# Performance work log

Hardware: AMD Instinct MI355X
Metric: run time of the kernel (lower is better)

The kernel has to match this reference:

```python
import jax, jax.numpy as jnp
import numpy as np

R = 256   # resolution
C = 16    # n_chan
F = 8     # n_freq
N = 262144


def setup_inputs() -> dict:
    key = jax.random.key(0)
    k1, k2 = jax.random.split(key)
    coords = jax.random.uniform(k1, (N, 3), dtype=jnp.float32, minval=-1.0, maxval=1.0)
    grid = jax.random.normal(k2, (3, C * F, R, R), dtype=jnp.float32) * 0.1
    # matches torch init: linspace(0,1,C*F).reshape(-1,C).T.reshape(-1)
    freqs = jnp.linspace(0.0, 1.0, C * F, dtype=jnp.float32).reshape(-1, C).T.reshape(-1)
    return {"coords": coords, "grid": grid, "freqs": freqs}


def _reflect(x, size):
    # PyTorch grid_sample reflection padding, align_corners=True:
    # reflect unnormalized coords about [0, size-1], period 2*(size-1)
    span = size - 1
    m = 2 * span
    r = jnp.abs(x) % m
    return jnp.where(r > span, m - r, r)


def _grid_sample_plane(img, xy):
    # img: (CF, R, R); xy: (Npts, 2) normalized [-1,1], (x indexes W, y indexes H)
    ix = _reflect((xy[:, 0] + 1.0) * 0.5 * (R - 1), R)
    iy = _reflect((xy[:, 1] + 1.0) * 0.5 * (R - 1), R)
    x0f = jnp.floor(ix); y0f = jnp.floor(iy)
    wx = ix - x0f; wy = iy - y0f
    x0 = jnp.clip(x0f.astype(jnp.int32), 0, R - 1)
    x1 = jnp.clip(x0 + 1, 0, R - 1)
    y0 = jnp.clip(y0f.astype(jnp.int32), 0, R - 1)
    y1 = jnp.clip(y0 + 1, 0, R - 1)
    v00 = img[:, y0, x0]  # (CF, Npts)
    v01 = img[:, y0, x1]
    v10 = img[:, y1, x0]
    v11 = img[:, y1, x1]
    return (v00 * (1 - wx) * (1 - wy) + v01 * wx * (1 - wy)
            + v10 * (1 - wx) * wy + v11 * wx * wy)


def reference(coords, grid, freqs):
    n = coords.shape[0]
    # tri-plane sample coords: plane0 (y,z), plane1 (x,z), plane2 (x,y)
    xy = jnp.stack([coords[:, (1, 2)], coords[:, (0, 2)], coords[:, (0, 1)]], 0)  # (3,N,2)
    coefs = jax.vmap(_grid_sample_plane)(grid, xy)          # (3, CF, N)
    coefs = coefs.transpose(2, 1, 0).reshape(n, C, F, 3)    # (N, C, F, 3)
    # get_freqs(): 2**(clamp(freqs,0,1)*log2(R)) - 1
    fr = 2.0 ** (jnp.clip(freqs, 0.0, 1.0) * np.float32(np.log2(R))) - 1.0  # (CF,)
    pts = (coords + 1.0) * 0.5 * (R - 1)                    # (N, 3)
    phase = (jnp.pi / R) * (pts[:, None, None, :] + 0.5) * (fr.reshape(C, F)[None, :, :, None] + 0.5)
    basis = jnp.cos(phase)                                   # (N, C, F, 3)
    # einsum BCFT,BCFT->BCT then sum over T == sum over (F, T)
    return 2.0 * jnp.sum(coefs * basis, axis=(2, 3))         # (N, C)
```

## Files before the change

### kernel.cpp

```cpp
#include <hip/hip_runtime.h>

#define RES   256
#define NCH   128
#define NC    16
#define QG    32
#define NPK   64
#define NBINS 4096
#define TBLK  3072

typedef float fx2 __attribute__((ext_vector_type(2)));

__device__ __forceinline__ unsigned int f32_to_bf16_rne(float f) {
    unsigned int u = __float_as_uint(f);
    return (u + 0x7FFFu + ((u >> 16) & 1u)) >> 16;
}
__device__ __forceinline__ float bf16_lo(unsigned int w) {
    return __uint_as_float(w << 16);
}
__device__ __forceinline__ float bf16_hi(unsigned int w) {
    return __uint_as_float(w & 0xFFFF0000u);
}
__device__ __forceinline__ float reflectf(float v) {
    float r = fabsf(v);
    r = fmodf(r, 510.0f);
    return (r > 255.0f) ? (510.0f - r) : r;
}
__device__ __forceinline__ unsigned spread3(unsigned v) {
    return (v & 1u) | ((v & 2u) << 2) | ((v & 4u) << 4) | ((v & 8u) << 6);
}
__device__ __forceinline__ int point_cell(const float* __restrict__ coords, int i) {
    const float r0 = reflectf((coords[3 * (size_t)i + 0] + 1.0f) * 127.5f);
    const float r1 = reflectf((coords[3 * (size_t)i + 1] + 1.0f) * 127.5f);
    const float r2 = reflectf((coords[3 * (size_t)i + 2] + 1.0f) * 127.5f);
    const unsigned cx = (unsigned)min(max((int)r0, 0), 255) >> 4;
    const unsigned cy = (unsigned)min(max((int)r1, 0), 255) >> 4;
    const unsigned cz = (unsigned)min(max((int)r2, 0), 255) >> 4;
    return (int)(spread3(cx) | (spread3(cy) << 1) | (spread3(cz) << 2));
}

__global__ __launch_bounds__(256) void fg_transpose_hist(
    const float* __restrict__ in, unsigned int* __restrict__ out,
    const float* __restrict__ coords, unsigned* __restrict__ hist, int n)
{
    __shared__ unsigned int tile[QG / 2][RES + 4];
    const int tid = threadIdx.x;
    const int qg = blockIdx.x;
    const int y  = blockIdx.y;
    const int p  = blockIdx.z;

    {
        const int bid = (p * RES + y) * 4 + qg;
        const int per = (n + TBLK - 1) / TBLK;
        const int s0 = bid * per;
        const int s1 = min(s0 + per, n);
        for (int k = s0 + tid; k < s1; k += 256)
            atomicAdd(&hist[point_cell(coords, k)], 1u);
    }

    const int q0 = qg * QG;
    const float* src = in + (((size_t)p * NCH + q0) * RES + y) * RES;
    #pragma unroll
    for (int it = 0; it < 4; ++it) {
        const int lin = it * 256 + tid;
        const int k   = lin >> 6;
        const int x4  = lin & 63;
        const float4 a = *(const float4*)(src + (size_t)(2 * k + 0) * (RES * RES) + x4 * 4);
        const float4 b = *(const float4*)(src + (size_t)(2 * k + 1) * (RES * RES) + x4 * 4);
        uint4 w;
        w.x = f32_to_bf16_rne(a.x) | (f32_to_bf16_rne(b.x) << 16);
        w.y = f32_to_bf16_rne(a.y) | (f32_to_bf16_rne(b.y) << 16);
        w.z = f32_to_bf16_rne(a.z) | (f32_to_bf16_rne(b.z) << 16);
        w.w = f32_to_bf16_rne(a.w) | (f32_to_bf16_rne(b.w) << 16);
        *(uint4*)&tile[k][x4 * 4] = w;
    }
    __syncthreads();
    unsigned int* dst = out + (((size_t)p * RES + y) * RES) * NPK + (q0 >> 1);
    #pragma unroll
    for (int it = 0; it < 4; ++it) {
        const int lin = it * 256 + tid;
        const int q4 = lin & 3;
        const int x  = lin >> 2;
        uint4 w;
        w.x = tile[4 * q4 + 0][x];
        w.y = tile[4 * q4 + 1][x];
        w.z = tile[4 * q4 + 2][x];
        w.w = tile[4 * q4 + 3][x];
        *(uint4*)&dst[(size_t)x * NPK + q4 * 4] = w;
    }
}

__global__ __launch_bounds__(256) void fg_scan(
    const unsigned* __restrict__ hist, unsigned* __restrict__ cursor,
    const float* __restrict__ freqs, float* __restrict__ frp)
{
    __shared__ unsigned wtot[4];
    const int t = threadIdx.x;
    const int lane = t & 63;
    const int wid = t >> 6;
    unsigned loc[16];
    unsigned sum = 0;
    #pragma unroll
    for (int k = 0; k < 16; ++k) { loc[k] = hist[t * 16 + k]; sum += loc[k]; }
    unsigned v = sum;
    #pragma unroll
    for (int off = 1; off < 64; off <<= 1) {
        unsigned u = __shfl_up(v, off);
        if (lane >= off) v += u;
    }
    if (lane == 63) wtot[wid] = v;
    __syncthreads();
    unsigned base = 0;
    #pragma unroll
    for (int w = 0; w < 4; ++w) base += (w < wid) ? wtot[w] : 0u;
    unsigned run = base + (v - sum);
    #pragma unroll
    for (int k = 0; k < 16; ++k) { cursor[t * 16 + k] = run; run += loc[k]; }
    if (t < 128) {
        const float f = fminf(fmaxf(freqs[t], 0.0f), 1.0f);
        frp[t] = __builtin_amdgcn_exp2f(f * 8.0f) - 0.5f;
    }
}

__global__ __launch_bounds__(256) void fg_scatter(
    const float* __restrict__ coords, unsigned* __restrict__ cursor,
    float4* __restrict__ recP, unsigned* __restrict__ idx, int n)
{
    const int i = blockIdx.x * 256 + threadIdx.x;
    if (i >= n) return;
    const float c0 = coords[3 * (size_t)i + 0];
    const float c1 = coords[3 * (size_t)i + 1];
    const float c2 = coords[3 * (size_t)i + 2];
    const float p0 = (c0 + 1.0f) * 127.5f;
    const float p1 = (c1 + 1.0f) * 127.5f;
    const float p2 = (c2 + 1.0f) * 127.5f;
    const float r0 = reflectf(p0);
    const float r1 = reflectf(p1);
    const float r2 = reflectf(p2);
    const unsigned cx = (unsigned)min(max((int)r0, 0), 255) >> 4;
    const unsigned cy = (unsigned)min(max((int)r1, 0), 255) >> 4;
    const unsigned cz = (unsigned)min(max((int)r2, 0), 255) >> 4;
    const int cell = (int)(spread3(cx) | (spread3(cy) << 1) | (spread3(cz) << 2));
    const unsigned pos = atomicAdd(&cursor[cell], 1u);

    #pragma unroll
    for (int p = 0; p < 3; ++p) {
        const float ix = (p == 0) ? r1 : r0;
        const float iy = (p == 2) ? r1 : r2;
        const float pp = (p == 0) ? p0 : ((p == 1) ? p1 : p2);
        const float x0f = floorf(ix), y0f = floorf(iy);
        const float wx = ix - x0f, wy = iy - y0f;
        const int x0 = min(max((int)x0f, 0), RES - 1);
        const int y0 = min(max((int)y0f, 0), RES - 1);
        unsigned ob = (unsigned)(((p << 16) | (y0 << 8) | x0) << 6);
        if (x0 < RES - 1) ob |= (1u << 24);
        if (y0 < RES - 1) ob |= (1u << 25);
        const float A = (pp + 0.5f) * (1.0f / 512.0f);
        recP[(size_t)pos * 3 + p] = make_float4(A, wx, wy, __uint_as_float(ob));
    }
    idx[pos] = (unsigned)i;
}

__global__ __launch_bounds__(256) void fg_main_bf16(
    const unsigned int* __restrict__ grid,
    const float* __restrict__ frp_in,
    const float4* __restrict__ recP,
    const unsigned* __restrict__ idx,
    float* __restrict__ out, int n)
{
    const int t = threadIdx.x;
    const int c = t & 15;
    int b = blockIdx.x;
    {
        const int G = gridDim.x;
        const int chunk = G >> 3;
        const int lim = chunk << 3;
        if (b < lim) b = (b & 7) * chunk + (b >> 3);
    }
    const int slot = b * 16 + (t >> 4);
    if (slot >= n) return;

    float4 P[3];
    P[0] = recP[(size_t)slot * 3 + 0];
    P[1] = recP[(size_t)slot * 3 + 1];
    P[2] = recP[(size_t)slot * 3 + 2];
    const unsigned i = idx[slot];

    fx2 frpv[4];
    {
        float frp[8];
        *(float4*)(frp + 0) = *(const float4*)(frp_in + c * 8 + 0);
        *(float4*)(frp + 4) = *(const float4*)(frp_in + c * 8 + 4);
        #pragma unroll
        for (int jj = 0; jj < 4; ++jj) {
            frpv[jj].x = frp[2 * jj + 0];
            frpv[jj].y = frp[2 * jj + 1];
        }
    }

    const int c4 = c * 4;
    uint4 g[3][4];
    #pragma unroll
    for (int p = 0; p < 3; ++p) {
        const unsigned bits = __float_as_uint(P[p].w);
        const int base = (int)(bits & 0x00FFFFFFu) + c4;
        const int dx = (int)((bits >> 18) & 64u);
        const int dy = (int)((bits >> 11) & 16384u);
        g[p][0] = *(const uint4*)(grid + base);
        g[p][1] = *(const uint4*)(grid + base + dx);
        g[p][2] = *(const uint4*)(grid + base + dy);
        g[p][3] = *(const uint4*)(grid + base + dx + dy);
    }

    fx2 acc2 = {0.0f, 0.0f};
    #pragma unroll
    for (int p = 0; p < 3; ++p) {
        const float wx = P[p].y, wy = P[p].z;
        const float u = 1.0f - wx, v = 1.0f - wy;
        const float w00 = u * v,  w01 = wx * v;
        const float w10 = u * wy, w11 = wx * wy;
        const float A = P[p].x;
        const unsigned int w0[4] = {g[p][0].x, g[p][0].y, g[p][0].z, g[p][0].w};
        const unsigned int w1[4] = {g[p][1].x, g[p][1].y, g[p][1].z, g[p][1].w};
        const unsigned int w2[4] = {g[p][2].x, g[p][2].y, g[p][2].z, g[p][2].w};
        const unsigned int w3[4] = {g[p][3].x, g[p][3].y, g[p][3].z, g[p][3].w};

        #pragma unroll
        for (int jj = 0; jj < 4; ++jj) {
            fx2 v0; v0.x = bf16_lo(w0[jj]); v0.y = bf16_hi(w0[jj]);
            fx2 v1; v1.x = bf16_lo(w1[jj]); v1.y = bf16_hi(w1[jj]);
            fx2 v2; v2.x = bf16_lo(w2[jj]); v2.y = bf16_hi(w2[jj]);
            fx2 v3; v3.x = bf16_lo(w3[jj]); v3.y = bf16_hi(w3[jj]);
            const fx2 cf = w00 * v0 + w01 * v1 + w10 * v2 + w11 * v3;
            fx2 ph = A * frpv[jj];
            ph.x = __builtin_amdgcn_fractf(ph.x);
            ph.y = __builtin_amdgcn_fractf(ph.y);
            fx2 cs;
            cs.x = __builtin_amdgcn_cosf(ph.x);
            cs.y = __builtin_amdgcn_cosf(ph.y);
            acc2 += cf * cs;
        }
    }

    __builtin_nontemporal_store(2.0f * (acc2.x + acc2.y), &out[(size_t)i * NC + c]);
}

__global__ __launch_bounds__(256) void fg_main_f32(
    const float* __restrict__ coords,
    const float* __restrict__ grid,
    const float* __restrict__ freqs,
    float* __restrict__ out, int n)
{
    const int t = threadIdx.x;
    const int c = t & 15;
    const int i = blockIdx.x * 16 + (t >> 4);
    if (i >= n) return;

    float frp[8];
    #pragma unroll
    for (int j = 0; j < 8; ++j) {
        float f = fminf(fmaxf(freqs[c * 8 + j], 0.0f), 1.0f);
        frp[j] = __builtin_amdgcn_exp2f(f * 8.0f) - 0.5f;
    }
    const float c0 = coords[3 * (size_t)i + 0];
    const float c1 = coords[3 * (size_t)i + 1];
    const float c2 = coords[3 * (size_t)i + 2];
    const float pts0 = (c0 + 1.0f) * 127.5f;
    const float pts1 = (c1 + 1.0f) * 127.5f;
    const float pts2 = (c2 + 1.0f) * 127.5f;
    float acc = 0.0f;
    #pragma unroll
    for (int p = 0; p < 3; ++p) {
        const float sx = (p == 0) ? pts1 : pts0;
        const float sy = (p == 2) ? pts1 : pts2;
        const float pp = (p == 0) ? pts0 : ((p == 1) ? pts1 : pts2);
        const float ix = reflectf(sx);
        const float iy = reflectf(sy);
        const float x0f = floorf(ix), y0f = floorf(iy);
        const float wx = ix - x0f, wy = iy - y0f;
        int x0 = (int)x0f; x0 = min(max(x0, 0), RES - 1);
        int y0 = (int)y0f; y0 = min(max(y0, 0), RES - 1);
        const int x1 = min(x0 + 1, RES - 1);
        const int y1 = min(y0 + 1, RES - 1);
        const float w00 = (1.0f - wx) * (1.0f - wy);
        const float w01 = wx * (1.0f - wy);
        const float w10 = (1.0f - wx) * wy;
        const float w11 = wx * wy;
        const float A = (pp + 0.5f) * (1.0f / 512.0f);
        const size_t plane = (size_t)p * NCH * RES * RES;
        const int o00 = y0 * RES + x0, o01 = y0 * RES + x1;
        const int o10 = y1 * RES + x0, o11 = y1 * RES + x1;
        #pragma unroll
        for (int j = 0; j < 8; ++j) {
            const float* gq = grid + plane + (size_t)(c * 8 + j) * (RES * RES);
            const float coef = w00 * gq[o00] + w01 * gq[o01]
                             + w10 * gq[o10] + w11 * gq[o11];
            const float rr = __builtin_amdgcn_fractf(A * frp[j]);
            acc += coef * __builtin_amdgcn_cosf(rr);
        }
    }
    out[(size_t)i * NC + c] = 2.0f * acc;
}

extern "C" void kernel_launch(void* const* d_in, const int* in_sizes, int n_in,
                              void* d_out, int out_size, void* d_ws, size_t ws_size,
                              hipStream_t stream)
{
    const float* coords = (const float*)d_in[0];
    const float* grid   = (const float*)d_in[1];
    const float* freqs  = (const float*)d_in[2];
    float* out = (float*)d_out;
    const int n = in_sizes[0] / 3;

    const size_t gridT_b  = (size_t)3 * RES * RES * NPK * sizeof(unsigned);
    const size_t hist_b   = (size_t)NBINS * sizeof(unsigned);
    const size_t frp_b    = 128 * sizeof(float);
    const size_t recP_b   = (size_t)n * 3 * sizeof(float4);
    const size_t idx_b    = (size_t)((n + 3) & ~3) * sizeof(unsigned);
    const size_t need = gridT_b + 2 * hist_b + frp_b + recP_b + idx_b;

    if (ws_size >= need) {
        char* ws = (char*)d_ws;
        unsigned* gridT  = (unsigned*)ws;                 ws += gridT_b;
        unsigned* hist   = (unsigned*)ws;                 ws += hist_b;
        unsigned* cursor = (unsigned*)ws;                 ws += hist_b;
        float*    frp    = (float*)ws;                    ws += frp_b;
        float4*   recP   = (float4*)ws;                   ws += recP_b;
        unsigned* idxb   = (unsigned*)ws;

        (void)hipMemsetAsync(hist, 0, hist_b, stream);
        hipLaunchKernelGGL(fg_transpose_hist, dim3(4, RES, 3), dim3(256), 0, stream,
                           grid, gridT, coords, hist, n);
        hipLaunchKernelGGL(fg_scan, dim3(1), dim3(256), 0, stream,
                           hist, cursor, freqs, frp);
        hipLaunchKernelGGL(fg_scatter, dim3((n + 255) / 256), dim3(256), 0, stream,
                           coords, cursor, recP, idxb, n);
        const int blocks = (n + 15) / 16;
        hipLaunchKernelGGL(fg_main_bf16, dim3(blocks), dim3(256), 0, stream,
                           gridT, frp, recP, idxb, out, n);
    } else {
        const int blocks = (n + 15) / 16;
        hipLaunchKernelGGL(fg_main_f32, dim3(blocks), dim3(256), 0, stream,
                           coords, grid, freqs, out, n);
    }
}
```

Measured before the change: 244.0 us.

## Repack bf16 grid as per-channel planar layout instead of texel-interleaved

Changes the packed bf16 grid layout from [plane][y][x][64 words] (all 128 channels per texel) to [plane][channel][y][x][4 words], so each channel's 8 frequencies are contiguous per texel. The pack kernel becomes a simple shared-memory-free gather of 8 strided floats per thread, with 12288 blocks, and the histogram work is spread over those blocks. The main kernel recomputes addresses per channel. Each thread's 16-byte loads now land in separate per-channel planes rather than one 256-byte texel record, which changes cache-line sharing across the 16 channel lanes of a point.

Measured after the change: 395.0 us. 1.62x slower.

```diff
diff --git a/kernel.cpp b/kernel.cpp
--- a/kernel.cpp
+++ b/kernel.cpp
@@ -3,10 +3,8 @@
 #define RES   256
 #define NCH   128
 #define NC    16
-#define QG    32
-#define NPK   64
 #define NBINS 4096
-#define TBLK  3072
+#define PBLK  12288
 
 typedef float fx2 __attribute__((ext_vector_type(2)));
 
@@ -38,55 +36,40 @@
     return (int)(spread3(cx) | (spread3(cy) << 1) | (spread3(cz) << 2));
 }
 
-__global__ __launch_bounds__(256) void fg_transpose_hist(
+__global__ __launch_bounds__(256) void fg_pack_hist(
     const float* __restrict__ in, unsigned int* __restrict__ out,
     const float* __restrict__ coords, unsigned* __restrict__ hist, int n)
 {
-    __shared__ unsigned int tile[QG / 2][RES + 4];
-    const int tid = threadIdx.x;
-    const int qg = blockIdx.x;
-    const int y  = blockIdx.y;
-    const int p  = blockIdx.z;
+    const int t = threadIdx.x;
+    const int b = blockIdx.x;
 
     {
-        const int bid = (p * RES + y) * 4 + qg;
-        const int per = (n + TBLK - 1) / TBLK;
-        const int s0 = bid * per;
+        const int per = (n + PBLK - 1) / PBLK;
+        const int s0 = b * per;
         const int s1 = min(s0 + per, n);
-        for (int k = s0 + tid; k < s1; k += 256)
+        for (int k = s0 + t; k < s1; k += 256)
             atomicAdd(&hist[point_cell(coords, k)], 1u);
     }
 
-    const int q0 = qg * QG;
-    const float* src = in + (((size_t)p * NCH + q0) * RES + y) * RES;
-    #pragma unroll
-    for (int it = 0; it < 4; ++it) {
-        const int lin = it * 256 + tid;
-        const int k   = lin >> 6;
-        const int x4  = lin & 63;
-        const float4 a = *(const float4*)(src + (size_t)(2 * k + 0) * (RES * RES) + x4 * 4);
-        const float4 b = *(const float4*)(src + (size_t)(2 * k + 1) * (RES * RES) + x4 * 4);
-        uint4 w;
-        w.x = f32_to_bf16_rne(a.x) | (f32_to_bf16_rne(b.x) << 16);
-        w.y = f32_to_bf16_rne(a.y) | (f32_to_bf16_rne(b.y) << 16);
-        w.z = f32_to_bf16_rne(a.z) | (f32_to_bf16_rne(b.z) << 16);
-        w.w = f32_to_bf16_rne(a.w) | (f32_to_bf16_rne(b.w) << 16);
-        *(uint4*)&tile[k][x4 * 4] = w;
-    }
-    __syncthreads();
-    unsigned int* dst = out + (((size_t)p * RES + y) * RES) * NPK + (q0 >> 1);
-    #pragma unroll
-    for (int it = 0; it < 4; ++it) {
-        const int lin = it * 256 + tid;
-        const int q4 = lin & 3;
-        const int x  = lin >> 2;
-        uint4 w;
-        w.x = tile[4 * q4 + 0][x];
-        w.y = tile[4 * q4 + 1][x];
-        w.z = tile[4 * q4 + 2][x];
-        w.w = tile[4 * q4 + 3][x];
-        *(uint4*)&dst[(size_t)x * NPK + q4 * 4] = w;
-    }
+    const int p = b >> 12;
+    const int c = (b >> 8) & 15;
+    const int y = b & 255;
+
+    const float* src = in + ((size_t)(p * NCH + c * 8) << 16) + y * 256 + t;
+    float q0 = src[0];
+    float q1 = src[(size_t)1 << 16];
+    float q2 = src[(size_t)2 << 16];
+    float q3 = src[(size_t)3 << 16];
+    float q4 = src[(size_t)4 << 16];
+    float q5 = src[(size_t)5 << 16];
+    float q6 = src[(size_t)6 << 16];
+    float q7 = src[(size_t)7 << 16];
+    uint4 w;
+    w.x = f32_to_bf16_rne(q0) | (f32_to_bf16_rne(q1) << 16);
+    w.y = f32_to_bf16_rne(q2) | (f32_to_bf16_rne(q3) << 16);
+    w.z = f32_to_bf16_rne(q4) | (f32_to_bf16_rne(q5) << 16);
+    w.w = f32_to_bf16_rne(q6) | (f32_to_bf16_rne(q7) << 16);
+    *(uint4*)(out + ((((size_t)(p * 16 + c)) << 16) + y * 256 + t) * 4) = w;
 }
 
 __global__ __launch_bounds__(256) void fg_scan(
@@ -151,7 +134,7 @@
         const float wx = ix - x0f, wy = iy - y0f;
         const int x0 = min(max((int)x0f, 0), RES - 1);
         const int y0 = min(max((int)y0f, 0), RES - 1);
-        unsigned ob = (unsigned)(((p << 16) | (y0 << 8) | x0) << 6);
+        unsigned ob = (unsigned)((y0 << 8) | x0);
         if (x0 < RES - 1) ob |= (1u << 24);
         if (y0 < RES - 1) ob |= (1u << 25);
         const float A = (pp + 0.5f) * (1.0f / 512.0f);
@@ -197,14 +180,14 @@
         }
     }
 
-    const int c4 = c * 4;
     uint4 g[3][4];
     #pragma unroll
     for (int p = 0; p < 3; ++p) {
         const unsigned bits = __float_as_uint(P[p].w);
-        const int base = (int)(bits & 0x00FFFFFFu) + c4;
-        const int dx = (int)((bits >> 18) & 64u);
-        const int dy = (int)((bits >> 11) & 16384u);
+        const int yx = (int)(bits & 0xFFFFu);
+        const int base = ((p * 16 + c) << 18) + (yx << 2);
+        const int dx = (int)((bits >> 22) & 4u);
+        const int dy = (int)((bits >> 15) & 1024u);
         g[p][0] = *(const uint4*)(grid + base);
         g[p][1] = *(const uint4*)(grid + base + dx);
         g[p][2] = *(const uint4*)(grid + base + dy);
@@ -311,7 +294,7 @@
     float* out = (float*)d_out;
     const int n = in_sizes[0] / 3;
 
-    const size_t gridT_b  = (size_t)3 * RES * RES * NPK * sizeof(unsigned);
+    const size_t gridT_b  = (size_t)3 * 16 * RES * RES * 4 * sizeof(unsigned);
     const size_t hist_b   = (size_t)NBINS * sizeof(unsigned);
     const size_t frp_b    = 128 * sizeof(float);
     const size_t recP_b   = (size_t)n * 3 * sizeof(float4);
@@ -328,7 +311,7 @@
         unsigned* idxb   = (unsigned*)ws;
 
         (void)hipMemsetAsync(hist, 0, hist_b, stream);
-        hipLaunchKernelGGL(fg_transpose_hist, dim3(4, RES, 3), dim3(256), 0, stream,
+        hipLaunchKernelGGL(fg_pack_hist, dim3(PBLK), dim3(256), 0, stream,
                            grid, gridT, coords, hist, n);
         hipLaunchKernelGGL(fg_scan, dim3(1), dim3(256), 0, stream,
                            hist, cursor, freqs, frp);
```
